# Kernel optimization log

Hardware: AMD Instinct MI355X
Metric: run time of the kernel (lower is better)

The kernel has to match this reference:

```python
import jax, jax.numpy as jnp
import numpy as np
from jax import lax

WS = 8  # window size

def conv1x1(x, W, b=None):
    y = jnp.einsum('bchw,oc->bohw', x, W)
    if b is not None:
        y = y + b[None, :, None, None]
    return y

def conv2d(x, W, b=None, dilation=1, groups=1):
    p = dilation * (W.shape[-1] // 2)
    y = lax.conv_general_dilated(x, W, (1, 1), [(p, p), (p, p)],
                                 rhs_dilation=(dilation, dilation),
                                 feature_group_count=groups,
                                 dimension_numbers=('NCHW', 'OIHW', 'NCHW'))
    if b is not None:
        y = y + b[None, :, None, None]
    return y

def ln_cf(x, w, b, eps=1e-6):
    # channels_first LayerNorm over channel dim
    u = x.mean(1, keepdims=True)
    s = ((x - u) ** 2).mean(1, keepdims=True)
    return w[None, :, None, None] * ((x - u) / jnp.sqrt(s + eps)) + b[None, :, None, None]

def to_windows(x):
    # b c (h dh) (w dw) -> b (h w) (dh dw c)
    B, C, H, W = x.shape
    h, w = H // WS, W // WS
    return x.reshape(B, C, h, WS, w, WS).transpose(0, 2, 4, 3, 5, 1).reshape(B, h * w, WS * WS * C)

def from_windows(x, C, H, W):
    B = x.shape[0]
    h, w = H // WS, W // WS
    return x.reshape(B, h, w, WS, WS, C).transpose(0, 5, 1, 3, 2, 4).reshape(B, C, H, W)

def lrelu(x):
    return jnp.where(x >= 0, x, 0.1 * x)

def gelu(x):
    return jax.nn.gelu(x, approximate=False)  # torch exact GELU

def _forward(x, w_norm1, b_norm1, w_norm2, b_norm2,
             Wv, bv, Wq, bq, Wk, bk, dw1, dwb1, dw2, dwb2, Wo, bo,
             W_in, b_in, Wc, bc, ln_w, ln_b, Wm1, bm1, Wm2, bm2,
             Wca, bca, Wsa, bsa, Wffn_in, dw_ffn, Wffn_out):
    B, C, H, W = x.shape
    ws2 = WS * WS
    N = (H // WS) * (W // WS)
    embed = ws2 * C
    # ---------- CAMixer ----------
    v = conv1x1(x, Wv, bv)
    # MaskPre routing
    xin = lrelu(conv1x1(v, W_in, b_in))                 # (B, C/4, H, W)
    x_ = lrelu(ln_cf(conv1x1(v, Wc, bc), ln_w, ln_b))   # (B, C/4, H, W)
    ca = jax.nn.sigmoid(conv1x1(x_.mean((2, 3), keepdims=True), Wca, bca))  # (B,C,1,1)
    sa = jax.nn.sigmoid(conv2d(x_, Wsa, bsa))           # (B,1,H,W)
    xm = to_windows(xin.mean(1, keepdims=True))         # (B,N,ws2)
    var = jnp.var(xm, axis=-1, ddof=1)                  # (B,N) torch.var unbiased
    k_top = N // 2
    _, idx = lax.top_k(-var, k_top)                     # bottom-k variance windows
    mbin = jnp.ones((B, N), x.dtype).at[jnp.arange(B)[:, None], idx].set(0.0)
    mfeat = jnp.broadcast_to(mbin[:, :, None], (B, N, embed))
    mask = lrelu(mfeat @ Wm1.T + bm1) @ Wm2.T + bm2     # (B,N,embed)
    # windowed content-routed attention
    vs = v * sa
    v_w, vs_w, x_w = to_windows(v), to_windows(vs), to_windows(x)
    v1 = (v_w * mask).reshape(B * N, ws2, C)
    v2 = vs_w * (1.0 - mask)
    t = (x_w * mask).reshape(B * N, ws2, C)             # masked q/k tokens (q=k=x)
    q1 = t @ Wq.T + bq
    k1 = t @ Wk.T + bk
    attn = jax.nn.softmax(q1 @ k1.transpose(0, 2, 1), axis=-1)  # (B*N, ws2, ws2)
    f = (attn @ v1).reshape(B, N, embed)
    img = from_windows(f + v2, C, H, W)
    cs = conv2d(conv2d(img, dw1, dwb1, 1, C), dw2, dwb2, 2, C)  # depthwise 3x3 + dilated
    out = gelu(cs) * ca + img
    res = conv1x1(out, Wo, bo)
    # ---------- norm1 + gated FFN + norm2 ----------
    x = ln_cf(x + res, w_norm1, b_norm1)
    y = conv2d(conv1x1(x, Wffn_in), dw_ffn, None, 1, 2 * C)
    y1, y2 = jnp.split(y, 2, axis=1)
    res = conv1x1(gelu(y1) * y2, Wffn_out)
    return ln_cf(x + res, w_norm2, b_norm2)

def setup_inputs():
    key = jax.random.key(0)
    B, C, H, W = 4, 64, 256, 256
    embed = WS * WS * C
    ks = iter(jax.random.split(key, 40))
    r = lambda *s: jax.random.normal(next(ks), s, jnp.float32) * 0.1
    return dict(
        x=jax.random.normal(next(ks), (B, C, H, W), jnp.float32),
        w_norm1=jnp.ones((C,), jnp.float32), b_norm1=jnp.zeros((C,), jnp.float32),
        w_norm2=jnp.ones((C,), jnp.float32), b_norm2=jnp.zeros((C,), jnp.float32),
        Wv=r(C, C), bv=r(C), Wq=r(C, C), bq=r(C), Wk=r(C, C), bk=r(C),
        dw1=r(C, 1, 3, 3), dwb1=r(C), dw2=r(C, 1, 3, 3), dwb2=r(C),
        Wo=r(C, C), bo=r(C),
        W_in=r(C // 4, C), b_in=r(C // 4), Wc=r(C // 4, C), bc=r(C // 4),
        ln_w=jnp.ones((C // 4,), jnp.float32), ln_b=jnp.zeros((C // 4,), jnp.float32),
        Wm1=r(embed // 2, embed) * 0.2, bm1=r(embed // 2),
        Wm2=r(embed, embed // 2) * 0.2, bm2=r(embed),
        Wca=r(C, C // 4), bca=r(C), Wsa=r(1, C // 4, 3, 3), bsa=r(1),
        Wffn_in=r(2 * C, C), dw_ffn=r(2 * C, 1, 3, 3), Wffn_out=r(C, C),
    )

def reference(x, w_norm1, b_norm1, w_norm2, b_norm2,
              Wv, bv, Wq, bq, Wk, bk, dw1, dwb1, dw2, dwb2, Wo, bo,
              W_in, b_in, Wc, bc, ln_w, ln_b, Wm1, bm1, Wm2, bm2,
              Wca, bca, Wsa, bsa, Wffn_in, dw_ffn, Wffn_out):
    return _forward(x, w_norm1, b_norm1, w_norm2, b_norm2,
                    Wv, bv, Wq, bq, Wk, bk, dw1, dwb1, dw2, dwb2, Wo, bo,
                    W_in, b_in, Wc, bc, ln_w, ln_b, Wm1, bm1, Wm2, bm2,
                    Wca, bca, Wsa, bsa, Wffn_in, dw_ffn, Wffn_out)
```

## Files before the change

### kernel.cpp

```cpp
#include <hip/hip_runtime.h>
#include <hip/hip_bf16.h>

typedef __hip_bfloat16 bf16;
typedef __attribute__((ext_vector_type(8))) short short8v;
typedef __attribute__((ext_vector_type(4))) float f32x4;

#define DEV static __device__ __forceinline__

DEV float b2f(bf16 h){ return __bfloat162float(h); }
DEV float us2f(unsigned short u){ unsigned v=((unsigned)u)<<16; float f; __builtin_memcpy(&f,&v,4); return f; }
DEV short f2bs(float f){ bf16 h=__float2bfloat16(f); short s; __builtin_memcpy(&s,&h,2); return s; }
DEV unsigned pack2(float a, float b){ return ((unsigned)(unsigned short)f2bs(b)<<16)|(unsigned short)f2bs(a); }
DEV float lrelu(float x){ return x >= 0.f ? x : 0.1f*x; }
DEV float geluf(float x){ return 0.5f*x*(1.f + erff(x*0.70710678118654752440f)); }
DEV float sigmoidf(float x){ return 1.f/(1.f + expf(-x)); }


__global__ __launch_bounds__(256) void k_detect(const void* x, int* flag){
  __shared__ int cnt;
  if(threadIdx.x==0) cnt=0;
  __syncthreads();
  const unsigned short* up=(const unsigned short*)x;
  int c=0;
  for(int k=0;k<16;k++){
    unsigned short u=up[(threadIdx.x*16+k)*2];
    if(((u>>7)&0xFF)==0xFF) c++;
  }
  atomicAdd(&cnt,c);
  __syncthreads();
  if(threadIdx.x==0) flag[0] = (cnt>0) ? 1 : 0;
}

struct CvtArgs { const void* src[31]; int sz[31]; int off[31]; };
__global__ __launch_bounds__(256) void k_cvt(CvtArgs a, const int* fl, float* wbuf){
  int t=blockIdx.x; int n=a.sz[t]; const void* s=a.src[t]; float* d=wbuf+a.off[t];
  if(fl[0]){
    const float* sp=(const float*)s;
    for(int i=threadIdx.x;i<n;i+=256) d[i]=sp[i];
  } else {
    const bf16* sp=(const bf16*)s;
    for(int i=threadIdx.x;i<n;i+=256) d[i]=b2f(sp[i]);
  }
}

__global__ __launch_bounds__(256) void k_w2b6(const float* __restrict__ wq, const float* __restrict__ wk,
    const float* __restrict__ wo, const float* __restrict__ wfi, const float* __restrict__ wfo,
    const float* __restrict__ wv,
    short* __restrict__ Wqb, short* __restrict__ Wkb,
    short* __restrict__ Wob, short* __restrict__ Wfib, short* __restrict__ Wfob,
    short* __restrict__ Wvb){
  int i=blockIdx.x*256+threadIdx.x;
  if(i<4096){ Wqb[i]=f2bs(wq[i]); Wkb[i]=f2bs(wk[i]); Wob[i]=f2bs(wo[i]); Wfob[i]=f2bs(wfo[i]); Wvb[i]=f2bs(wv[i]); }
  if(i<8192) Wfib[i]=f2bs(wfi[i]);
}

__global__ __launch_bounds__(256) void k_wcomp(const float* __restrict__ W_in, const float* __restrict__ b_in,
    const float* __restrict__ Wc, const float* __restrict__ bc,
    const float* __restrict__ Wv, const float* __restrict__ bv,
    float* __restrict__ Wa, float* __restrict__ ba,
    float* __restrict__ Wb2, float* __restrict__ bb2){
  int t=threadIdx.x;
  #pragma unroll
  for(int ii=0;ii<4;ii++){
    int idx=t+ii*256;
    int i=idx>>6, c=idx&63;
    float sa=0.f, sb=0.f;
    for(int k=0;k<64;k++){
      float wv=Wv[k*64+c];
      sa+=W_in[i*64+k]*wv;
      sb+=Wc[i*64+k]*wv;
    }
    Wa[idx]=sa; Wb2[idx]=sb;
  }
  if(t<16){
    float sa=0.f, sb=0.f;
    for(int k=0;k<64;k++){ sa+=W_in[t*64+k]*bv[k]; sb+=Wc[t*64+k]*bv[k]; }
    ba[t]=sa+b_in[t]; bb2[t]=sb+bc[t];
  }
}

__global__ __launch_bounds__(256) void k_convv_mf(
    const void* __restrict__ in, const int* __restrict__ fl,
    const short* __restrict__ Wvb, const float* __restrict__ bv,
    unsigned short* __restrict__ vw){
  __shared__ short Ain[64*72];
  int tid=threadIdx.x;
  int g0=blockIdx.x*64; int b=g0>>16, p0=g0&65535;
  int c=tid>>2, q=tid&3;
  size_t base=(((size_t)(b*64+c))<<16) + p0;
  if(fl[0]){
    const float* ip=(const float*)in + base;
    #pragma unroll
    for(int j=0;j<4;j++){
      int po=q*16+j*4;
      float4 xv=*(const float4*)(ip+po);
      Ain[(po+0)*72+c]=f2bs(xv.x); Ain[(po+1)*72+c]=f2bs(xv.y);
      Ain[(po+2)*72+c]=f2bs(xv.z); Ain[(po+3)*72+c]=f2bs(xv.w);
    }
  } else {
    const unsigned short* ip=(const unsigned short*)in + base;
    #pragma unroll
    for(int j=0;j<4;j++){
      int po=q*16+j*4;
      uint2 u=*(const uint2*)(ip+po);
      Ain[(po+0)*72+c]=(short)(u.x&0xffff); Ain[(po+1)*72+c]=(short)(u.x>>16);
      Ain[(po+2)*72+c]=(short)(u.y&0xffff); Ain[(po+3)*72+c]=(short)(u.y>>16);
    }
  }
  __syncthreads();
  int lane=tid&63, wid=tid>>6;
  int lr=lane&15, lg=lane>>4;
  int pix0=wid*16;
  short8v bfrag[2];
  #pragma unroll
  for(int ks=0;ks<2;ks++) bfrag[ks]=*(const short8v*)&Ain[(pix0+lr)*72 + ks*32 + lg*8];
  int y=p0>>8;
  int xx=(p0&255)+pix0+lr;
  int n=((y>>3)<<5)|(xx>>3), tok=((y&7)<<3)|(xx&7);
  unsigned short* wp=vw + (((size_t)(b*1024+n))<<12) + tok;
  #pragma unroll
  for(int nt=0;nt<4;nt++){
    f32x4 acc;
    #pragma unroll
    for(int r=0;r<4;r++) acc[r]=bv[nt*16+lg*4+r];
    #pragma unroll
    for(int ks=0;ks<2;ks++){
      short8v afrag=*(const short8v*)(Wvb + (nt*16+lr)*64 + ks*32 + lg*8);
      acc=__builtin_amdgcn_mfma_f32_16x16x32_bf16(afrag,bfrag[ks],acc,0,0,0);
    }
    #pragma unroll
    for(int r=0;r<4;r++){
      int m=nt*16+lg*4+r;
      wp[(size_t)m*64]=(unsigned short)f2bs(acc[r]);
    }
  }
}

__global__ __launch_bounds__(256) void k_gemm_mf(
    const void* __restrict__ in, int in_f32,
    const short* __restrict__ Wb, const float* __restrict__ bias, int has_bias,
    void* __restrict__ out, int och, int out_bf16){
  __shared__ short Ain[64*72];
  int tid=threadIdx.x;
  int g0=blockIdx.x*64; int b=g0>>16, p0=g0&65535;
  int c=tid>>2, q=tid&3;
  size_t base=(((size_t)(b*64+c))<<16) + p0;
  if(in_f32){
    const float* ip=(const float*)in + base;
    #pragma unroll
    for(int j=0;j<4;j++){
      int po=q*16+j*4;
      float4 xv=*(const float4*)(ip+po);
      Ain[(po+0)*72+c]=f2bs(xv.x); Ain[(po+1)*72+c]=f2bs(xv.y);
      Ain[(po+2)*72+c]=f2bs(xv.z); Ain[(po+3)*72+c]=f2bs(xv.w);
    }
  } else {
    const unsigned short* ip=(const unsigned short*)in + base;
    #pragma unroll
    for(int j=0;j<4;j++){
      int po=q*16+j*4;
      uint2 u=*(const uint2*)(ip+po);
      Ain[(po+0)*72+c]=(short)(u.x&0xffff); Ain[(po+1)*72+c]=(short)(u.x>>16);
      Ain[(po+2)*72+c]=(short)(u.y&0xffff); Ain[(po+3)*72+c]=(short)(u.y>>16);
    }
  }
  __syncthreads();
  int lane=tid&63, wid=tid>>6;
  int lr=lane&15, lg=lane>>4;
  int pix0=wid*16;
  short8v bfrag[2];
  #pragma unroll
  for(int ks=0;ks<2;ks++) bfrag[ks]=*(const short8v*)&Ain[(pix0+lr)*72 + ks*32 + lg*8];
  int ntn=och>>4;
  for(int nt=0;nt<ntn;nt++){
    f32x4 acc;
    if(has_bias){
      #pragma unroll
      for(int r=0;r<4;r++) acc[r]=bias[nt*16+lg*4+r];
    } else {
      acc=(f32x4){0.f,0.f,0.f,0.f};
    }
    #pragma unroll
    for(int ks=0;ks<2;ks++){
      short8v afrag=*(const short8v*)(Wb + (nt*16+lr)*64 + ks*32 + lg*8);
      acc=__builtin_amdgcn_mfma_f32_16x16x32_bf16(afrag,bfrag[ks],acc,0,0,0);
    }
    if(out_bf16){
      unsigned short* op=(unsigned short*)out;
      #pragma unroll
      for(int r=0;r<4;r++){
        int m=nt*16+lg*4+r;
        op[(((size_t)(b*och+m))<<16) + p0 + pix0 + lr]=(unsigned short)f2bs(acc[r]);
      }
    } else {
      float* op=(float*)out;
      #pragma unroll
      for(int r=0;r<4;r++){
        int m=nt*16+lg*4+r;
        op[(((size_t)(b*och+m))<<16) + p0 + pix0 + lr]=acc[r];
      }
    }
  }
}

__global__ __launch_bounds__(256) void k_gemm_ln(
    const unsigned short* __restrict__ in,
    const short* __restrict__ Wb, const float* __restrict__ bias, int has_bias,
    const void* __restrict__ basex,
    const float* __restrict__ lnw, const float* __restrict__ lnb,
    void* __restrict__ out,
    const int* __restrict__ fl, int base_mode, int out_mode){
  __shared__ short Ain[64*72];
  int tid=threadIdx.x;
  int g0=blockIdx.x*64; int b=g0>>16, p0=g0&65535;
  int c=tid>>2, q=tid&3;
  {
    const unsigned short* ip=in + (((size_t)(b*64+c))<<16) + p0;
    #pragma unroll
    for(int j=0;j<4;j++){
      int po=q*16+j*4;
      uint2 u=*(const uint2*)(ip+po);
      Ain[(po+0)*72+c]=(short)(u.x&0xffff); Ain[(po+1)*72+c]=(short)(u.x>>16);
      Ain[(po+2)*72+c]=(short)(u.y&0xffff); Ain[(po+3)*72+c]=(short)(u.y>>16);
    }
  }
  __syncthreads();
  int lane=tid&63, wid=tid>>6;
  int lr=lane&15, lg=lane>>4;
  int pix0=wid*16;
  short8v bfrag[2];
  #pragma unroll
  for(int ks=0;ks<2;ks++) bfrag[ks]=*(const short8v*)&Ain[(pix0+lr)*72 + ks*32 + lg*8];
  float rl[16];
  #pragma unroll
  for(int nt=0;nt<4;nt++){
    f32x4 acc;
    if(has_bias){
      #pragma unroll
      for(int r=0;r<4;r++) acc[r]=bias[nt*16+lg*4+r];
    } else {
      acc=(f32x4){0.f,0.f,0.f,0.f};
    }
    #pragma unroll
    for(int ks=0;ks<2;ks++){
      short8v afrag=*(const short8v*)(Wb + (nt*16+lr)*64 + ks*32 + lg*8);
      acc=__builtin_amdgcn_mfma_f32_16x16x32_bf16(afrag,bfrag[ks],acc,0,0,0);
    }
    #pragma unroll
    for(int r=0;r<4;r++) rl[nt*4+r]=acc[r];
  }
  int pix=p0+pix0+lr;
  bool bf32 = (base_mode==1) || (base_mode==0 && fl[0]);
  if(bf32){
    const float* xp=(const float*)basex;
    #pragma unroll
    for(int nt=0;nt<4;nt++)
      #pragma unroll
      for(int r=0;r<4;r++)
        rl[nt*4+r]+=xp[(((size_t)(b*64+nt*16+lg*4+r))<<16)+pix];
  } else {
    const unsigned short* xp=(const unsigned short*)basex;
    #pragma unroll
    for(int nt=0;nt<4;nt++)
      #pragma unroll
      for(int r=0;r<4;r++)
        rl[nt*4+r]+=us2f(xp[(((size_t)(b*64+nt*16+lg*4+r))<<16)+pix]);
  }
  float s=0.f;
  #pragma unroll
  for(int i=0;i<16;i++) s+=rl[i];
  s+=__shfl_xor(s,16); s+=__shfl_xor(s,32);
  float mean=s*(1.f/64.f);
  float qv=0.f;
  #pragma unroll
  for(int i=0;i<16;i++){ float d=rl[i]-mean; qv+=d*d; }
  qv+=__shfl_xor(qv,16); qv+=__shfl_xor(qv,32);
  float inv=1.f/sqrtf(qv*(1.f/64.f)+1e-6f);
  bool of32 = (out_mode==1) || (out_mode==0 && fl[0]);
  if(of32){
    float* op=(float*)out;
    #pragma unroll
    for(int nt=0;nt<4;nt++)
      #pragma unroll
      for(int r=0;r<4;r++){
        int m=nt*16+lg*4+r;
        op[(((size_t)(b*64+m))<<16)+pix]=lnw[m]*((rl[nt*4+r]-mean)*inv)+lnb[m];
      }
  } else {
    unsigned short* op=(unsigned short*)out;
    #pragma unroll
    for(int nt=0;nt<4;nt++)
      #pragma unroll
      for(int r=0;r<4;r++){
        int m=nt*16+lg*4+r;
        op[(((size_t)(b*64+m))<<16)+pix]=(unsigned short)f2bs(lnw[m]*((rl[nt*4+r]-mean)*inv)+lnb[m]);
      }
  }
}

__global__ __launch_bounds__(256) void k_route(const void* __restrict__ x, const int* __restrict__ fl,
    const float* __restrict__ Wa, const float* __restrict__ ba,
    const float* __restrict__ Wb2, const float* __restrict__ bb2,
    const float* __restrict__ lnw, const float* __restrict__ lnb,
    float* __restrict__ x_, float* __restrict__ xm, float* __restrict__ capart){
  __shared__ float wA[1024], wB[1024], sba[16], sbb[16], slw[16], slb[16];
  __shared__ float sred[4][16];
  int tid=threadIdx.x;
  for(int i=tid;i<1024;i+=256){ wA[i]=Wa[i]; wB[i]=Wb2[i]; }
  if(tid<16){ sba[tid]=ba[tid]; sbb[tid]=bb2[tid]; slw[tid]=lnw[tid]; slb[tid]=lnb[tid]; }
  __syncthreads();
  int g=blockIdx.x*512+tid*2; int b=g>>16, p=g&65535;
  float2 aA[16], aB[16];
  #pragma unroll
  for(int i=0;i<16;i++){ aA[i]=make_float2(sba[i],sba[i]); aB[i]=make_float2(sbb[i],sbb[i]); }
  size_t base=(((size_t)b*64)<<16)+p;
  if(fl[0]){
    const float* vp=(const float*)x+base;
    for(int c=0;c<64;c++){
      float2 vv=*(const float2*)(vp+(((size_t)c)<<16));
      #pragma unroll
      for(int i=0;i<16;i++){
        float wa=wA[(i<<6)+c], wb=wB[(i<<6)+c];
        aA[i].x+=wa*vv.x; aA[i].y+=wa*vv.y;
        aB[i].x+=wb*vv.x; aB[i].y+=wb*vv.y;
      }
    }
  } else {
    const unsigned short* vp=(const unsigned short*)x+base;
    for(int c=0;c<64;c++){
      unsigned u=*(const unsigned*)(vp+(((size_t)c)<<16));
      float v0=us2f(u&0xffff), v1=us2f(u>>16);
      #pragma unroll
      for(int i=0;i<16;i++){
        float wa=wA[(i<<6)+c], wb=wB[(i<<6)+c];
        aA[i].x+=wa*v0; aA[i].y+=wa*v1;
        aB[i].x+=wb*v0; aB[i].y+=wb*v1;
      }
    }
  }
  float s0=0.f,s1=0.f;
  #pragma unroll
  for(int i=0;i<16;i++){ aA[i].x=lrelu(aA[i].x); aA[i].y=lrelu(aA[i].y); s0+=aA[i].x; s1+=aA[i].y; }
  float2 xmst; xmst.x=s0*(1.f/16.f); xmst.y=s1*(1.f/16.f);
  *(float2*)(xm+g)=xmst;
  float u0=0.f,u1=0.f;
  #pragma unroll
  for(int i=0;i<16;i++){ u0+=aB[i].x; u1+=aB[i].y; }
  u0*=(1.f/16.f); u1*=(1.f/16.f);
  float q0=0.f,q1=0.f;
  #pragma unroll
  for(int i=0;i<16;i++){ float d0=aB[i].x-u0, d1=aB[i].y-u1; q0+=d0*d0; q1+=d1*d1; }
  q0*=(1.f/16.f); q1*=(1.f/16.f);
  float i0=1.f/sqrtf(q0+1e-6f), i1=1.f/sqrtf(q1+1e-6f);
  float red[16];
  float* xp=x_+(((size_t)b*16)<<16)+p;
  #pragma unroll
  for(int i=0;i<16;i++){
    float xv0=lrelu(slw[i]*((aB[i].x-u0)*i0)+slb[i]);
    float xv1=lrelu(slw[i]*((aB[i].y-u1)*i1)+slb[i]);
    float2 st; st.x=xv0; st.y=xv1;
    *(float2*)(xp+(((size_t)i)<<16))=st;
    red[i]=xv0+xv1;
  }
  int lane=tid&63, wid=tid>>6;
  #pragma unroll
  for(int i=0;i<16;i++){
    float val=red[i];
    for(int m=32;m>0;m>>=1) val+=__shfl_xor(val,m);
    if(lane==0) sred[wid][i]=val;
  }
  __syncthreads();
  if(tid<16) capart[blockIdx.x*16+tid]=sred[0][tid]+sred[1][tid]+sred[2][tid]+sred[3][tid];
}

__global__ __launch_bounds__(256) void k_sa(const float* __restrict__ x_,
    const float* __restrict__ Wsa, const float* __restrict__ bsa, unsigned short* __restrict__ sa_w){
  __shared__ float w[144]; __shared__ float bb;
  int tid=threadIdx.x;
  if(tid<144) w[tid]=Wsa[tid];
  if(tid==0) bb=bsa[0];
  __syncthreads();
  int pix=blockIdx.x*256+tid; int b=pix>>16, p=pix&65535;
  int y=p>>8, xx=p&255;
  float acc=bb;
  #pragma unroll
  for(int i=0;i<16;i++){
    const float* pl=x_+(((size_t)(b*16+i))<<16);
    #pragma unroll
    for(int ky=0;ky<3;ky++){
      int yy=y+ky-1;
      if((unsigned)yy<256u){
        #pragma unroll
        for(int kx=0;kx<3;kx++){
          int x2=xx+kx-1;
          if((unsigned)x2<256u) acc+=pl[(yy<<8)+x2]*w[i*9+ky*3+kx];
        }
      }
    }
  }
  int n=((y>>3)<<5)|(xx>>3), tok=((y&7)<<3)|(xx&7);
  sa_w[(((size_t)(b<<10)+n)<<6)+tok]=(unsigned short)f2bs(sigmoidf(acc));
}

__global__ __launch_bounds__(64) void k_var(const float* __restrict__ xm, float* __restrict__ var){
  int blk=blockIdx.x, tid=threadIdx.x;
  int b=blk>>10, n=blk&1023;
  int pix=((n>>5)<<11) + ((n&31)<<3) + ((tid>>3)<<8) + (tid&7);
  float val=xm[(b<<16)+pix];
  float s=val;
  for(int m=32;m>0;m>>=1) s+=__shfl_xor(s,m);
  float mean=s*(1.f/64.f);
  float d=val-mean; float q=d*d;
  for(int m=32;m>0;m>>=1) q+=__shfl_xor(q,m);
  if(tid==0) var[blk]=q*(1.f/63.f);
}

__global__ __launch_bounds__(256) void k_rank(const float* __restrict__ var, float* __restrict__ mbin){
  __shared__ float va[1024];
  int bid=blockIdx.x; int b=bid>>2, seg=bid&3;
  int tid=threadIdx.x;
  for(int i=tid;i<1024;i+=256) va[i]=var[(b<<10)+i];
  __syncthreads();
  int n=seg*256+tid;
  float vn=va[n]; int r=0;
  for(int m=0;m<1024;m++){ float vm=va[m]; r += (vm<vn) || (vm==vn && m<n); }
  mbin[(b<<10)+n] = (r<512)?0.f:1.f;
}

__global__ __launch_bounds__(64) void k_hvec(const void* __restrict__ Wm1, const float* __restrict__ bm1,
    float* __restrict__ h0, float* __restrict__ h1, const int* __restrict__ fl){
  int j=blockIdx.x, tid=threadIdx.x;
  float s=0.f;
  if(fl[0]){
    const float* row=(const float*)Wm1+((size_t)j<<12);
    for(int k=tid;k<4096;k+=64) s+=row[k];
  } else {
    const bf16* row=(const bf16*)Wm1+((size_t)j<<12);
    for(int k=tid;k<4096;k+=64) s+=b2f(row[k]);
  }
  for(int m=32;m>0;m>>=1) s+=__shfl_xor(s,m);
  if(tid==0){ float bb=bm1[j]; h0[j]=lrelu(bb); h1[j]=lrelu(bb+s); }
}

__global__ __launch_bounds__(64) void k_mask(const void* __restrict__ Wm2, const float* __restrict__ bm2,
    const float* __restrict__ h0, const float* __restrict__ h1,
    float* __restrict__ m0, float* __restrict__ m1,
    float* __restrict__ m0T, float* __restrict__ m1T, const int* __restrict__ fl){
  int e=blockIdx.x, tid=threadIdx.x;
  float p0=0.f,p1=0.f;
  if(fl[0]){
    const float* row=(const float*)Wm2+((size_t)e<<11);
    for(int j=tid;j<2048;j+=64){ float w=row[j]; p0+=w*h0[j]; p1+=w*h1[j]; }
  } else {
    const bf16* row=(const bf16*)Wm2+((size_t)e<<11);
    for(int j=tid;j<2048;j+=64){ float w=b2f(row[j]); p0+=w*h0[j]; p1+=w*h1[j]; }
  }
  for(int m=32;m>0;m>>=1){ p0+=__shfl_xor(p0,m); p1+=__shfl_xor(p1,m); }
  if(tid==0){
    float bb=bm2[e]; float v0=p0+bb, v1=p1+bb;
    m0[e]=v0; m1[e]=v1;
    int te=(e&63)*64+(e>>6);
    m0T[te]=v0; m1T[te]=v1;
  }
}

__global__ __launch_bounds__(64) void k_ca(const float* __restrict__ capart,
    const float* __restrict__ Wca, const float* __restrict__ bca, float* __restrict__ ca){
  __shared__ float m[16];
  int b=blockIdx.x, tid=threadIdx.x;
  if(tid<16){
    float s=0.f;
    for(int blk=0;blk<128;blk++) s+=capart[((b*128)+blk)*16+tid];
    m[tid]=s*(1.f/65536.f);
  }
  __syncthreads();
  float a=bca[tid];
  #pragma unroll
  for(int i=0;i<16;i++) a+=Wca[(tid<<4)+i]*m[i];
  ca[(b<<6)+tid]=sigmoidf(a);
}

__global__ __launch_bounds__(256) void k_pack_x(const void* __restrict__ x,
    const float* __restrict__ mbin, const float* __restrict__ m0T, const float* __restrict__ m1T,
    const int* __restrict__ fl, unsigned short* __restrict__ xwb){
  __shared__ unsigned short sW[2*64*72];
  int wp=blockIdx.x; int b=wp>>9, np=wp&511;
  int n0=np*2;
  int base=((n0>>5)<<11)+((n0&31)<<3);
  int t=threadIdx.x; int ch0=t&31, row=t>>5;
  int isf32=fl[0];
  const float* mTa = (mbin[b*1024+n0  ]>0.5f)? m1T : m0T;
  const float* mTb = (mbin[b*1024+n0+1]>0.5f)? m1T : m0T;
  for(int h=0;h<2;h++){
    int ch=ch0+h*32;
    size_t gb=(((size_t)(b*64+ch))<<16) + base + row*256;
    float xv[16];
    if(isf32){
      const float* xp=(const float*)x+gb;
      #pragma unroll
      for(int i=0;i<16;i++) xv[i]=xp[i];
    } else {
      const bf16* xp=(const bf16*)x+gb;
      #pragma unroll
      for(int i=0;i<16;i++) xv[i]=b2f(xp[i]);
    }
    #pragma unroll
    for(int wnd=0;wnd<2;wnd++){
      const float* mT = wnd? mTb : mTa;
      int s=wnd*8;
      #pragma unroll
      for(int j=0;j<8;j++){
        float mk=mT[ch*64+row*8+j];
        sW[wnd*4608 + (row*8+j)*72 + ch]=(unsigned short)f2bs(xv[s+j]*mk);
      }
    }
  }
  __syncthreads();
  size_t ob=((size_t)(b*1024+n0))<<12;
  #pragma unroll
  for(int k2=0;k2<4;k2++){
    int idx=t+k2*256; int win=idx>>9, rem=idx&511, tok=rem>>3, cg=rem&7;
    uint4 val=*(const uint4*)&sW[win*4608 + tok*72 + cg*8];
    *(uint4*)(xwb + ob + (size_t)win*4096 + tok*64 + cg*8)=val;
  }
}

#define STR 72
#define STRF 65
__global__ __launch_bounds__(256) void k_attn_mfma(
    const unsigned short* __restrict__ xwb, const unsigned short* __restrict__ vw,
    const unsigned short* __restrict__ sa_w, const float* __restrict__ mbin,
    const float* __restrict__ m0T, const float* __restrict__ m1T,
    const short* __restrict__ Wqb, const float* __restrict__ bq,
    const short* __restrict__ Wkb, const float* __restrict__ bk,
    unsigned short* __restrict__ img){
  __shared__ short sQK[2*64*STR];
  __shared__ short sV1[64*STR];
  __shared__ float ssa[64];
  short* sQ=sQK; short* sK=sQK+64*STR;
  float* sF=(float*)sQK;
  int tid=threadIdx.x, blk=blockIdx.x;
  int b=blk>>10, n=blk&1023;
  int base=((n>>5)<<11) + ((n&31)<<3);
  size_t plane=((size_t)b*64)<<16;
  const float* mT = (mbin[blk]>0.5f)? m1T : m0T;
  const unsigned short* xw=xwb+(size_t)blk*4096;
  const unsigned short* vw2=vw+(size_t)blk*4096;
  if(tid<64) ssa[tid]=us2f(sa_w[((size_t)blk<<6)+tid]);
  for(int task=tid;task<512;task+=256){
    int c=task>>3, tok0=(task&7)*8;
    uint4 uv=*(const uint4*)(vw2 + c*64 + tok0);
    float4 ma=*(const float4*)(mT + c*64 + tok0);
    float4 mb=*(const float4*)(mT + c*64 + tok0 + 4);
    uint4 o;
    o.x=pack2(us2f(uv.x&0xffff)*ma.x, us2f(uv.x>>16)*ma.y);
    o.y=pack2(us2f(uv.y&0xffff)*ma.z, us2f(uv.y>>16)*ma.w);
    o.z=pack2(us2f(uv.z&0xffff)*mb.x, us2f(uv.z>>16)*mb.y);
    o.w=pack2(us2f(uv.w&0xffff)*mb.z, us2f(uv.w>>16)*mb.w);
    *(uint4*)&sV1[c*STR+tok0]=o;
  }
  int lane=tid&63, wid=tid>>6;
  int pb=wid*16, lr=lane&15, lg=lane>>4;
  short8v ta[2];
  #pragma unroll
  for(int ks=0;ks<2;ks++) ta[ks]=*(const short8v*)(xw + (pb+lr)*64 + ks*32 + lg*8);
  #pragma unroll
  for(int nt=0;nt<4;nt++){
    float bqv=bq[nt*16+lr], bkv=bk[nt*16+lr];
    f32x4 qa={bqv,bqv,bqv,bqv}, ka={bkv,bkv,bkv,bkv};
    #pragma unroll
    for(int ks=0;ks<2;ks++){
      short8v wq=*(const short8v*)(Wqb + (nt*16+lr)*64 + ks*32 + lg*8);
      short8v wk=*(const short8v*)(Wkb + (nt*16+lr)*64 + ks*32 + lg*8);
      qa=__builtin_amdgcn_mfma_f32_16x16x32_bf16(ta[ks],wq,qa,0,0,0);
      ka=__builtin_amdgcn_mfma_f32_16x16x32_bf16(ta[ks],wk,ka,0,0,0);
    }
    #pragma unroll
    for(int r=0;r<4;r++){
      sQ[(pb+lg*4+r)*STR + nt*16+lr]=f2bs(qa[r]);
      sK[(pb+lg*4+r)*STR + nt*16+lr]=f2bs(ka[r]);
    }
  }
  __syncthreads();
  short8v qa2[2];
  #pragma unroll
  for(int ks=0;ks<2;ks++) qa2[ks]=*(const short8v*)&sQ[(pb+lr)*STR + ks*32 + lg*8];
  f32x4 sacc[4];
  #pragma unroll
  for(int nt=0;nt<4;nt++){
    f32x4 a={0.f,0.f,0.f,0.f};
    #pragma unroll
    for(int ks=0;ks<2;ks++){
      short8v kb=*(const short8v*)&sK[(nt*16+lr)*STR + ks*32 + lg*8];
      a=__builtin_amdgcn_mfma_f32_16x16x32_bf16(qa2[ks],kb,a,0,0,0);
    }
    sacc[nt]=a;
  }
  f32x4 pa[4];
  #pragma unroll
  for(int r=0;r<4;r++){
    float mx=fmaxf(fmaxf(sacc[0][r],sacc[1][r]),fmaxf(sacc[2][r],sacc[3][r]));
    #pragma unroll
    for(int m=1;m<16;m<<=1) mx=fmaxf(mx,__shfl_xor(mx,m));
    float e0=__expf(sacc[0][r]-mx), e1=__expf(sacc[1][r]-mx);
    float e2=__expf(sacc[2][r]-mx), e3=__expf(sacc[3][r]-mx);
    float sum=e0+e1+e2+e3;
    #pragma unroll
    for(int m=1;m<16;m<<=1) sum+=__shfl_xor(sum,m);
    float inv=1.f/sum;
    pa[0][r]=e0*inv; pa[1][r]=e1*inv; pa[2][r]=e2*inv; pa[3][r]=e3*inv;
  }
  #pragma unroll
  for(int nt=0;nt<4;nt++){
    #pragma unroll
    for(int r=0;r<4;r++)
      sQ[(pb+lg*4+r)*STR + nt*16+lr]=f2bs(pa[nt][r]);
  }
  short8v aa[2];
  #pragma unroll
  for(int ks=0;ks<2;ks++) aa[ks]=*(const short8v*)&sQ[(pb+lr)*STR + ks*32 + lg*8];
  __syncthreads();
  #pragma unroll
  for(int nt=0;nt<4;nt++){
    f32x4 f={0.f,0.f,0.f,0.f};
    #pragma unroll
    for(int ks=0;ks<2;ks++){
      short8v vb=*(const short8v*)&sV1[(nt*16+lr)*STR + ks*32 + lg*8];
      f=__builtin_amdgcn_mfma_f32_16x16x32_bf16(aa[ks],vb,f,0,0,0);
    }
    #pragma unroll
    for(int r=0;r<4;r++) sF[(pb+lg*4+r)*STRF + nt*16+lr]=f[r];
  }
  __syncthreads();
  for(int e2=tid;e2<2048;e2+=256){
    int c=e2>>5, tp=e2&31; int tok=tp*2;
    float f0=sF[tok*STRF+c], f1=sF[(tok+1)*STRF+c];
    unsigned uv=*(const unsigned*)(vw2 + c*64 + tok);
    float mk0=mT[c*64+tok], mk1=mT[c*64+tok+1];
    float vs0=us2f(uv&0xffff)*ssa[tok]*(1.f-mk0);
    float vs1=us2f(uv>>16)*ssa[tok+1]*(1.f-mk1);
    int pix=base+((tok>>3)<<8)+(tok&7);
    *(unsigned*)(img+plane+(((size_t)c)<<16)+pix)=pack2(f0+vs0, f1+vs1);
  }
}

#define DWI 264
__global__ __launch_bounds__(256) void k_dwfuse(const unsigned short* __restrict__ img,
    const float* __restrict__ dw1w, const float* __restrict__ dwb1,
    const float* __restrict__ dw2w, const float* __restrict__ dwb2,
    const float* __restrict__ ca, unsigned short* __restrict__ outb){
  __shared__ float sImg[22*DWI];
  __shared__ float sTmp[20*DWI];
  __shared__ float k1[9], k2[9];
  __shared__ float bb1, bb2, cav;
  int bid=blockIdx.x; int b=bid>>10, c=(bid>>4)&63, sy=bid&15;
  int y0=sy*16;
  int tid=threadIdx.x;
  if(tid<9){ k1[tid]=dw1w[c*9+tid]; k2[tid]=dw2w[c*9+tid]; }
  if(tid==9)  bb1=dwb1[c];
  if(tid==10) bb2=dwb2[c];
  if(tid==11) cav=ca[b*64+c];
  const unsigned short* ip=img+(((size_t)(b*64+c))<<16);
  for(int task=tid;task<1452;task+=256){
    int r=task/66, j=task-r*66;
    int gy=y0-3+r, gx0=4*j-4;
    float4 v=make_float4(0.f,0.f,0.f,0.f);
    if((unsigned)gy<256u && j>=1 && j<=64){
      uint2 u=*(const uint2*)(ip+(gy<<8)+gx0);
      v.x=us2f(u.x&0xffff); v.y=us2f(u.x>>16); v.z=us2f(u.y&0xffff); v.w=us2f(u.y>>16);
    }
    *(float4*)&sImg[r*DWI+4*j]=v;
  }
  __syncthreads();
  for(int task=tid;task<1300;task+=256){
    int r=task/65, g=task-r*65;
    int ty=y0-2+r, tc0=4*g-2;
    float t[4]={bb1,bb1,bb1,bb1};
    #pragma unroll
    for(int dy=0;dy<3;dy++){
      float4 A0=*(const float4*)&sImg[(r+dy)*DWI+4*g];
      float4 A1=*(const float4*)&sImg[(r+dy)*DWI+4*g+4];
      float F[8]={A0.x,A0.y,A0.z,A0.w,A1.x,A1.y,A1.z,A1.w};
      #pragma unroll
      for(int dx=0;dx<3;dx++){
        float kk=k1[dy*3+dx];
        #pragma unroll
        for(int e=0;e<4;e++) t[e]+=F[1+e+dx]*kk;
      }
    }
    float4 res;
    bool rowok=((unsigned)ty<256u);
    #pragma unroll
    for(int e=0;e<4;e++){
      int tc=tc0+e;
      ((float*)&res)[e]= (rowok && (unsigned)tc<256u)? t[e] : 0.f;
    }
    *(float4*)&sTmp[r*DWI+4*g]=res;
  }
  __syncthreads();
  int q=tid&63, rr=tid>>6;
  unsigned short* op=outb+(((size_t)(b*64+c))<<16);
  #pragma unroll
  for(int l4=0;l4<4;l4++){
    int ly=rr*4+l4;
    float cs[4]={bb2,bb2,bb2,bb2};
    #pragma unroll
    for(int dy=0;dy<3;dy++){
      int r=ly+2*dy;
      float4 T0=*(const float4*)&sTmp[r*DWI+4*q];
      float4 T1=*(const float4*)&sTmp[r*DWI+4*q+4];
      float T[8]={T0.x,T0.y,T0.z,T0.w,T1.x,T1.y,T1.z,T1.w};
      #pragma unroll
      for(int dx=0;dx<3;dx++){
        float kk=k2[dy*3+dx];
        #pragma unroll
        for(int e=0;e<4;e++) cs[e]+=T[e+2*dx]*kk;
      }
    }
    float4 C=*(const float4*)&sImg[(ly+3)*DWI+4*q+4];
    float o0=geluf(cs[0])*cav+C.x;
    float o1=geluf(cs[1])*cav+C.y;
    float o2=geluf(cs[2])*cav+C.z;
    float o3=geluf(cs[3])*cav+C.w;
    uint2 u; u.x=pack2(o0,o1); u.y=pack2(o2,o3);
    *(uint2*)(op+((y0+ly)<<8)+4*q)=u;
  }
}

#define FEI 264
__global__ __launch_bounds__(256) void k_ffn_dw_t(const unsigned short* __restrict__ E,
    const float* __restrict__ dwf, unsigned short* __restrict__ g){
  __shared__ unsigned short sE1[18*FEI];
  __shared__ unsigned short sE2[18*FEI];
  __shared__ float k1[9], k2[9];
  int bid=blockIdx.x; int b=bid>>10, c=(bid>>4)&63, sy=bid&15;
  int y0=sy*16;
  int tid=threadIdx.x;
  if(tid<9){ k1[tid]=dwf[c*9+tid]; k2[tid]=dwf[(64+c)*9+tid]; }
  const unsigned short* p1=E+(((size_t)(b*128+c))<<16);
  const unsigned short* p2=E+(((size_t)(b*128+64+c))<<16);
  for(int task=tid;task<1188;task+=256){
    int r=task/66, j=task-r*66;
    int gy=y0-1+r, gx0=4*j-4;
    uint2 u1=make_uint2(0,0), u2=make_uint2(0,0);
    if((unsigned)gy<256u && j>=1 && j<=64){
      u1=*(const uint2*)(p1+(gy<<8)+gx0);
      u2=*(const uint2*)(p2+(gy<<8)+gx0);
    }
    *(uint2*)&sE1[r*FEI+4*j]=u1;
    *(uint2*)&sE2[r*FEI+4*j]=u2;
  }
  __syncthreads();
  int q=tid&63, rr=tid>>6;
  unsigned short* op=g+(((size_t)(b*64+c))<<16);
  #pragma unroll
  for(int l4=0;l4<4;l4++){
    int ly=rr*4+l4;
    float a1[4]={0.f,0.f,0.f,0.f}, a2[4]={0.f,0.f,0.f,0.f};
    #pragma unroll
    for(int dy=0;dy<3;dy++){
      int r=ly+dy;
      unsigned w0=*(const unsigned*)&sE1[r*FEI+4*q+2];
      uint2   w1=*(const uint2*)  &sE1[r*FEI+4*q+4];
      unsigned w2=*(const unsigned*)&sE1[r*FEI+4*q+8];
      float GA[6]={us2f(w0>>16),us2f(w1.x&0xffff),us2f(w1.x>>16),us2f(w1.y&0xffff),us2f(w1.y>>16),us2f(w2&0xffff)};
      unsigned v0=*(const unsigned*)&sE2[r*FEI+4*q+2];
      uint2   v1=*(const uint2*)  &sE2[r*FEI+4*q+4];
      unsigned v2=*(const unsigned*)&sE2[r*FEI+4*q+8];
      float GB[6]={us2f(v0>>16),us2f(v1.x&0xffff),us2f(v1.x>>16),us2f(v1.y&0xffff),us2f(v1.y>>16),us2f(v2&0xffff)};
      #pragma unroll
      for(int dx=0;dx<3;dx++){
        float ka=k1[dy*3+dx], kb=k2[dy*3+dx];
        #pragma unroll
        for(int e=0;e<4;e++){
          a1[e]+=GA[e+dx]*ka;
          a2[e]+=GB[e+dx]*kb;
        }
      }
    }
    float o0=geluf(a1[0])*a2[0];
    float o1=geluf(a1[1])*a2[1];
    float o2=geluf(a1[2])*a2[2];
    float o3=geluf(a1[3])*a2[3];
    uint2 u; u.x=pack2(o0,o1); u.y=pack2(o2,o3);
    *(uint2*)(op+((y0+ly)<<8)+4*q)=u;
  }
}

extern "C" void kernel_launch(void* const* d_in, const int* in_sizes, int n_in,
                              void* d_out, int out_size, void* d_ws, size_t ws_size,
                              hipStream_t stream){
  (void)in_sizes; (void)n_in; (void)out_size; (void)ws_size;
  const void* x  = d_in[0];
  const void* Wm1= d_in[23];
  const void* Wm2= d_in[25];

  char* ws=(char*)d_ws;
  unsigned short* E=(unsigned short*)(ws);
  unsigned short* img=(unsigned short*)(ws+67108864);
  unsigned short* x1b=(unsigned short*)(ws+67108864);
  unsigned short* xwb=(unsigned short*)(ws+134217728);
  unsigned short* outb=(unsigned short*)(ws+134217728);
  unsigned short* gbuf=(unsigned short*)(ws+134217728);
  unsigned short* vw =(unsigned short*)(ws+230686720);
  char* sm = ws+201326592;
  float* x_    =(float*)(sm);
  unsigned short* sa_w=(unsigned short*)(sm+16777216);
  float* xm    =(float*)(sm+17825792);
  float* var   =(float*)(sm+18874368);
  float* mbin  =(float*)(sm+18890752);
  float* h0    =(float*)(sm+18907136);
  float* h1    =(float*)(sm+18915328);
  float* m0    =(float*)(sm+18923520);
  float* m1    =(float*)(sm+18939904);
  float* capart=(float*)(sm+18956288);
  float* ca    =(float*)(sm+19021824);
  int*   flag  =(int*)  (sm+19022848);
  float* wbuf  =(float*)(sm+19023872);
  short* Wqb   =(short*)(sm+19200000);
  short* Wkb   =(short*)(sm+19208192);
  float* m0T   =(float*)(sm+19216384);
  float* m1T   =(float*)(sm+19232768);
  short* Wob   =(short*)(sm+19249152);
  short* Wfib  =(short*)(sm+19257344);
  short* Wfob  =(short*)(sm+19273728);
  short* Wvb   =(short*)(sm+19281920);
  float* WaC   =(float*)(sm+19290112);
  float* WbC   =(float*)(sm+19294208);
  float* baC   =(float*)(sm+19298304);
  float* bbC   =(float*)(sm+19298560);

  static const int din_idx[31]={5,6,7,8,9,10,11,12,13,14,15,16,17,18,19,20,21,22,24,26,27,28,29,30,31,32,33,1,2,3,4};
  static const int szs[31]  ={4096,64,4096,64,4096,64,576,64,576,64,4096,64,1024,16,1024,16,16,16,2048,4096,1024,64,144,1,8192,1152,4096,64,64,64,64};
  CvtArgs ca_args;
  int off=0;
  int offs[31];
  for(int t=0;t<31;t++){
    ca_args.src[t]=d_in[din_idx[t]];
    ca_args.sz[t]=szs[t];
    ca_args.off[t]=off;
    offs[t]=off;
    off+=szs[t];
  }
  const float* Wv  =wbuf+offs[0];  const float* bv  =wbuf+offs[1];
  const float* Wq  =wbuf+offs[2];  const float* bq  =wbuf+offs[3];
  const float* Wk  =wbuf+offs[4];  const float* bk  =wbuf+offs[5];
  const float* dw1 =wbuf+offs[6];  const float* dwb1=wbuf+offs[7];
  const float* dw2 =wbuf+offs[8];  const float* dwb2=wbuf+offs[9];
  const float* Wo  =wbuf+offs[10]; const float* bo  =wbuf+offs[11];
  const float* W_in=wbuf+offs[12]; const float* b_in=wbuf+offs[13];
  const float* Wc  =wbuf+offs[14]; const float* bc  =wbuf+offs[15];
  const float* lnw =wbuf+offs[16]; const float* lnb =wbuf+offs[17];
  const float* bm1 =wbuf+offs[18]; const float* bm2 =wbuf+offs[19];
  const float* Wca =wbuf+offs[20]; const float* bca =wbuf+offs[21];
  const float* Wsa =wbuf+offs[22]; const float* bsa =wbuf+offs[23];
  const float* Wfi =wbuf+offs[24]; const float* dwf =wbuf+offs[25];
  const float* Wfo =wbuf+offs[26];
  const float* wn1 =wbuf+offs[27]; const float* bn1 =wbuf+offs[28];
  const float* wn2 =wbuf+offs[29]; const float* bn2 =wbuf+offs[30];

  hipLaunchKernelGGL(k_detect,   dim3(1),      dim3(256), 0, stream, x, flag);
  hipLaunchKernelGGL(k_cvt,      dim3(31),     dim3(256), 0, stream, ca_args, flag, wbuf);
  hipLaunchKernelGGL(k_w2b6,     dim3(32),     dim3(256), 0, stream, Wq, Wk, Wo, Wfi, Wfo, Wv, Wqb, Wkb, Wob, Wfib, Wfob, Wvb);
  hipLaunchKernelGGL(k_wcomp,    dim3(1),      dim3(256), 0, stream, W_in, b_in, Wc, bc, Wv, bv, WaC, baC, WbC, bbC);
  hipLaunchKernelGGL(k_convv_mf, dim3(4096),   dim3(256), 0, stream, x, flag, Wvb, bv, vw);
  hipLaunchKernelGGL(k_route,    dim3(512),    dim3(256), 0, stream, x, flag, WaC, baC, WbC, bbC, lnw, lnb, x_, xm, capart);
  hipLaunchKernelGGL(k_sa,       dim3(1024),   dim3(256), 0, stream, x_, Wsa, bsa, sa_w);
  hipLaunchKernelGGL(k_var,      dim3(4096),   dim3(64),  0, stream, xm, var);
  hipLaunchKernelGGL(k_rank,     dim3(16),     dim3(256), 0, stream, var, mbin);
  hipLaunchKernelGGL(k_hvec,     dim3(2048),   dim3(64),  0, stream, Wm1, bm1, h0, h1, flag);
  hipLaunchKernelGGL(k_mask,     dim3(4096),   dim3(64),  0, stream, Wm2, bm2, h0, h1, m0, m1, m0T, m1T, flag);
  hipLaunchKernelGGL(k_ca,       dim3(4),      dim3(64),  0, stream, capart, Wca, bca, ca);
  hipLaunchKernelGGL(k_pack_x,   dim3(2048),   dim3(256), 0, stream, x, mbin, m0T, m1T, flag, xwb);
  hipLaunchKernelGGL(k_attn_mfma,dim3(4096),   dim3(256), 0, stream, xwb, vw, sa_w, mbin, m0T, m1T, Wqb, bq, Wkb, bk, img);
  hipLaunchKernelGGL(k_dwfuse,   dim3(4096),   dim3(256), 0, stream, img, dw1, dwb1, dw2, dwb2, ca, outb);
  hipLaunchKernelGGL(k_gemm_ln,  dim3(4096),   dim3(256), 0, stream, outb, Wob, bo, 1, x, wn1, bn1, (void*)x1b, flag, 0, 2);
  hipLaunchKernelGGL(k_gemm_mf,  dim3(4096),   dim3(256), 0, stream, (const void*)x1b, 0, Wfib, wbuf, 0, (void*)E, 128, 1);
  hipLaunchKernelGGL(k_ffn_dw_t, dim3(4096),   dim3(256), 0, stream, E, dwf, gbuf);
  hipLaunchKernelGGL(k_gemm_ln,  dim3(4096),   dim3(256), 0, stream, gbuf, Wfob, wbuf, 0, (const void*)x1b, wn2, bn2, d_out, flag, 2, 0);
}
```

Before: 508.3 us.

## Fuse masked window packing into the v-conv kernel and prefetch attention epilogue operands

The masked-x window packing (formerly k_pack_x) now runs inside k_convv_mf, which is moved after the mask computation. Both outputs come from one shared-memory tile of x, so x is read from global memory once instead of twice and one launch is removed. The tile is now stored as fp32 in channel-major order, which adds per-element bf16 conversion and strided LDS reads when building MFMA fragments. Separately, the attention epilogue now loads v and mask values into registers before the barrier, so their latency overlaps the preceding MFMA work.

```diff
diff --git a/kernel.cpp b/kernel.cpp
--- a/kernel.cpp
+++ b/kernel.cpp
@@ -82,8 +82,9 @@
 __global__ __launch_bounds__(256) void k_convv_mf(
     const void* __restrict__ in, const int* __restrict__ fl,
     const short* __restrict__ Wvb, const float* __restrict__ bv,
-    unsigned short* __restrict__ vw){
-  __shared__ short Ain[64*72];
+    const float* __restrict__ mbin, const float* __restrict__ m0T, const float* __restrict__ m1T,
+    unsigned short* __restrict__ vw, unsigned short* __restrict__ xwb){
+  __shared__ float Xf[64*66];
   int tid=threadIdx.x;
   int g0=blockIdx.x*64; int b=g0>>16, p0=g0&65535;
   int c=tid>>2, q=tid&3;
@@ -94,8 +95,8 @@
     for(int j=0;j<4;j++){
       int po=q*16+j*4;
       float4 xv=*(const float4*)(ip+po);
-      Ain[(po+0)*72+c]=f2bs(xv.x); Ain[(po+1)*72+c]=f2bs(xv.y);
-      Ain[(po+2)*72+c]=f2bs(xv.z); Ain[(po+3)*72+c]=f2bs(xv.w);
+      *(float2*)&Xf[c*66+po]=make_float2(xv.x,xv.y);
+      *(float2*)&Xf[c*66+po+2]=make_float2(xv.z,xv.w);
     }
   } else {
     const unsigned short* ip=(const unsigned short*)in + base;
@@ -103,8 +104,8 @@
     for(int j=0;j<4;j++){
       int po=q*16+j*4;
       uint2 u=*(const uint2*)(ip+po);
-      Ain[(po+0)*72+c]=(short)(u.x&0xffff); Ain[(po+1)*72+c]=(short)(u.x>>16);
-      Ain[(po+2)*72+c]=(short)(u.y&0xffff); Ain[(po+3)*72+c]=(short)(u.y>>16);
+      *(float2*)&Xf[c*66+po]=make_float2(us2f(u.x&0xffff),us2f(u.x>>16));
+      *(float2*)&Xf[c*66+po+2]=make_float2(us2f(u.y&0xffff),us2f(u.y>>16));
     }
   }
   __syncthreads();
@@ -113,7 +114,12 @@
   int pix0=wid*16;
   short8v bfrag[2];
   #pragma unroll
-  for(int ks=0;ks<2;ks++) bfrag[ks]=*(const short8v*)&Ain[(pix0+lr)*72 + ks*32 + lg*8];
+  for(int ks=0;ks<2;ks++){
+    short8v v;
+    #pragma unroll
+    for(int i=0;i<8;i++) v[i]=f2bs(Xf[(ks*32+lg*8+i)*66 + pix0+lr]);
+    bfrag[ks]=v;
+  }
   int y=p0>>8;
   int xx=(p0&255)+pix0+lr;
   int n=((y>>3)<<5)|(xx>>3), tok=((y&7)<<3)|(xx&7);
@@ -133,6 +139,27 @@
       int m=nt*16+lg*4+r;
       wp[(size_t)m*64]=(unsigned short)f2bs(acc[r]);
     }
+  }
+  int nw0=((y>>3)<<5) | ((p0&255)>>3);
+  int trow=(y&7)*8;
+  #pragma unroll
+  for(int k2=0;k2<2;k2++){
+    int task=tid+k2*256;
+    int w=task>>6, rem=task&63, j=rem>>3, cg=rem&7;
+    int nn=nw0+w;
+    const float* mT=(mbin[b*1024+nn]>0.5f)? m1T : m0T;
+    int tk=trow+j;
+    int pixl=w*8+j;
+    unsigned short ov[8];
+    #pragma unroll
+    for(int i=0;i<8;i++){
+      int ch=cg*8+i;
+      ov[i]=(unsigned short)f2bs(Xf[ch*66+pixl]*mT[ch*64+tk]);
+    }
+    uint4 o;
+    o.x=((unsigned)ov[1]<<16)|ov[0]; o.y=((unsigned)ov[3]<<16)|ov[2];
+    o.z=((unsigned)ov[5]<<16)|ov[4]; o.w=((unsigned)ov[7]<<16)|ov[6];
+    *(uint4*)(xwb + (((size_t)(b*1024+nn))<<12) + tk*64 + cg*8)=o;
   }
 }
 
@@ -478,51 +505,6 @@
   #pragma unroll
   for(int i=0;i<16;i++) a+=Wca[(tid<<4)+i]*m[i];
   ca[(b<<6)+tid]=sigmoidf(a);
-}
-
-__global__ __launch_bounds__(256) void k_pack_x(const void* __restrict__ x,
-    const float* __restrict__ mbin, const float* __restrict__ m0T, const float* __restrict__ m1T,
-    const int* __restrict__ fl, unsigned short* __restrict__ xwb){
-  __shared__ unsigned short sW[2*64*72];
-  int wp=blockIdx.x; int b=wp>>9, np=wp&511;
-  int n0=np*2;
-  int base=((n0>>5)<<11)+((n0&31)<<3);
-  int t=threadIdx.x; int ch0=t&31, row=t>>5;
-  int isf32=fl[0];
-  const float* mTa = (mbin[b*1024+n0  ]>0.5f)? m1T : m0T;
-  const float* mTb = (mbin[b*1024+n0+1]>0.5f)? m1T : m0T;
-  for(int h=0;h<2;h++){
-    int ch=ch0+h*32;
-    size_t gb=(((size_t)(b*64+ch))<<16) + base + row*256;
-    float xv[16];
-    if(isf32){
-      const float* xp=(const float*)x+gb;
-      #pragma unroll
-      for(int i=0;i<16;i++) xv[i]=xp[i];
-    } else {
-      const bf16* xp=(const bf16*)x+gb;
-      #pragma unroll
-      for(int i=0;i<16;i++) xv[i]=b2f(xp[i]);
-    }
-    #pragma unroll
-    for(int wnd=0;wnd<2;wnd++){
-      const float* mT = wnd? mTb : mTa;
-      int s=wnd*8;
-      #pragma unroll
-      for(int j=0;j<8;j++){
-        float mk=mT[ch*64+row*8+j];
-        sW[wnd*4608 + (row*8+j)*72 + ch]=(unsigned short)f2bs(xv[s+j]*mk);
-      }
-    }
-  }
-  __syncthreads();
-  size_t ob=((size_t)(b*1024+n0))<<12;
-  #pragma unroll
-  for(int k2=0;k2<4;k2++){
-    int idx=t+k2*256; int win=idx>>9, rem=idx&511, tok=rem>>3, cg=rem&7;
-    uint4 val=*(const uint4*)&sW[win*4608 + tok*72 + cg*8];
-    *(uint4*)(xwb + ob + (size_t)win*4096 + tok*64 + cg*8)=val;
-  }
 }
 
 #define STR 72
@@ -619,6 +601,14 @@
   short8v aa[2];
   #pragma unroll
   for(int ks=0;ks<2;ks++) aa[ks]=*(const short8v*)&sQ[(pb+lr)*STR + ks*32 + lg*8];
+  unsigned pvv[8]; float pm0[8], pm1[8];
+  #pragma unroll
+  for(int it=0;it<8;it++){
+    int e2=tid+it*256;
+    int cc=e2>>5, tp=e2&31; int tok=tp*2;
+    pvv[it]=*(const unsigned*)(vw2 + cc*64 + tok);
+    pm0[it]=mT[cc*64+tok]; pm1[it]=mT[cc*64+tok+1];
+  }
   __syncthreads();
   #pragma unroll
   for(int nt=0;nt<4;nt++){
@@ -632,15 +622,15 @@
     for(int r=0;r<4;r++) sF[(pb+lg*4+r)*STRF + nt*16+lr]=f[r];
   }
   __syncthreads();
-  for(int e2=tid;e2<2048;e2+=256){
-    int c=e2>>5, tp=e2&31; int tok=tp*2;
-    float f0=sF[tok*STRF+c], f1=sF[(tok+1)*STRF+c];
-    unsigned uv=*(const unsigned*)(vw2 + c*64 + tok);
-    float mk0=mT[c*64+tok], mk1=mT[c*64+tok+1];
-    float vs0=us2f(uv&0xffff)*ssa[tok]*(1.f-mk0);
-    float vs1=us2f(uv>>16)*ssa[tok+1]*(1.f-mk1);
+  #pragma unroll
+  for(int it=0;it<8;it++){
+    int e2=tid+it*256;
+    int cc=e2>>5, tp=e2&31; int tok=tp*2;
+    float f0=sF[tok*STRF+cc], f1=sF[(tok+1)*STRF+cc];
+    float vs0=us2f(pvv[it]&0xffff)*ssa[tok]*(1.f-pm0[it]);
+    float vs1=us2f(pvv[it]>>16)*ssa[tok+1]*(1.f-pm1[it]);
     int pix=base+((tok>>3)<<8)+(tok&7);
-    *(unsigned*)(img+plane+(((size_t)c)<<16)+pix)=pack2(f0+vs0, f1+vs1);
+    *(unsigned*)(img+plane+(((size_t)cc)<<16)+pix)=pack2(f0+vs0, f1+vs1);
   }
 }
 
@@ -863,7 +853,6 @@
   hipLaunchKernelGGL(k_cvt,      dim3(31),     dim3(256), 0, stream, ca_args, flag, wbuf);
   hipLaunchKernelGGL(k_w2b6,     dim3(32),     dim3(256), 0, stream, Wq, Wk, Wo, Wfi, Wfo, Wv, Wqb, Wkb, Wob, Wfib, Wfob, Wvb);
   hipLaunchKernelGGL(k_wcomp,    dim3(1),      dim3(256), 0, stream, W_in, b_in, Wc, bc, Wv, bv, WaC, baC, WbC, bbC);
-  hipLaunchKernelGGL(k_convv_mf, dim3(4096),   dim3(256), 0, stream, x, flag, Wvb, bv, vw);
   hipLaunchKernelGGL(k_route,    dim3(512),    dim3(256), 0, stream, x, flag, WaC, baC, WbC, bbC, lnw, lnb, x_, xm, capart);
   hipLaunchKernelGGL(k_sa,       dim3(1024),   dim3(256), 0, stream, x_, Wsa, bsa, sa_w);
   hipLaunchKernelGGL(k_var,      dim3(4096),   dim3(64),  0, stream, xm, var);
@@ -871,7 +860,7 @@
   hipLaunchKernelGGL(k_hvec,     dim3(2048),   dim3(64),  0, stream, Wm1, bm1, h0, h1, flag);
   hipLaunchKernelGGL(k_mask,     dim3(4096),   dim3(64),  0, stream, Wm2, bm2, h0, h1, m0, m1, m0T, m1T, flag);
   hipLaunchKernelGGL(k_ca,       dim3(4),      dim3(64),  0, stream, capart, Wca, bca, ca);
-  hipLaunchKernelGGL(k_pack_x,   dim3(2048),   dim3(256), 0, stream, x, mbin, m0T, m1T, flag, xwb);
+  hipLaunchKernelGGL(k_convv_mf, dim3(4096),   dim3(256), 0, stream, x, flag, Wvb, bv, mbin, m0T, m1T, vw, xwb);
   hipLaunchKernelGGL(k_attn_mfma,dim3(4096),   dim3(256), 0, stream, xwb, vw, sa_w, mbin, m0T, m1T, Wqb, bq, Wkb, bk, img);
   hipLaunchKernelGGL(k_dwfuse,   dim3(4096),   dim3(256), 0, stream, img, dw1, dwb1, dw2, dwb2, ca, outb);
   hipLaunchKernelGGL(k_gemm_ln,  dim3(4096),   dim3(256), 0, stream, outb, Wob, bo, 1, x, wn1, bn1, (void*)x1b, flag, 0, 2);
```

Measured after the change: 493.9 us. 2.8% less time.
